# Performance work log

Measured on AMD Instinct MI355X. Metric: run time of the kernel, lower is better.

The kernel has to match this reference:

```python
import jax, jax.numpy as jnp
import numpy as np

DM = 512; DS = 16; DC = 4; DI = 1024; DI4 = 256; K = 5; NL = 2; TEMP = 0.5
B = 4; N = 1024
L4 = 2 * NL  # 2 forward layers + 2 reverse layers, stacked on leading dim


def setup_inputs() -> dict:
    key = jax.random.key(0)
    ks = jax.random.split(key, 12)
    g = lambda k, shp: jax.random.normal(k, shp, dtype=jnp.float32) * 0.02
    A0 = jnp.log(jnp.arange(1, DS + 1, dtype=jnp.float32))  # (DS,)
    return {
        "x": jax.random.normal(ks[0], (B, N, DM), dtype=jnp.float32),
        "centers_init": g(ks[1], (K, DM)),
        "in_w": g(ks[2], (L4, DM, 2 * DI)),
        "conv_w": g(ks[3], (L4, DI, DC)),
        "conv_b": jnp.zeros((L4, DI), jnp.float32),
        "xp_w": g(ks[4], (L4, DI, 2 * DS + 1)),
        "dt_w": g(ks[5], (L4, DI)),
        "dt_b": jnp.zeros((L4, DI), jnp.float32),
        "cm_w1": g(ks[6], (L4, DI4)),
        "cm_b1": jnp.zeros((L4, DI4), jnp.float32),
        "cm_w2": g(ks[7], (L4, DI4, DI)),
        "cm_b2": jnp.zeros((L4, DI), jnp.float32),
        "A_log": jnp.tile(A0[None, None, :], (L4, DI, 1)),
        "D_p": jnp.ones((L4, DI), jnp.float32),
        "out_w": g(ks[8], (L4, DI, DM)),
        "ln_g": jnp.ones((L4, DM), jnp.float32),
        "ln_b": jnp.zeros((L4, DM), jnp.float32),
        "fusion_w": g(ks[9], (2 * DM, DM)),
        "fusion_b": jnp.zeros((DM,), jnp.float32),
        "fn_g": jnp.ones((DM,), jnp.float32),
        "fn_b": jnp.zeros((DM,), jnp.float32),
    }


def _layer_norm(x, g, b, eps=1e-5):
    mu = jnp.mean(x, axis=-1, keepdims=True)
    var = jnp.mean((x - mu) ** 2, axis=-1, keepdims=True)
    return (x - mu) * jax.lax.rsqrt(var + eps) * g + b


def _cdist(a, b):
    # (B,N,C) x (B,K,C) -> (B,N,K); tiny eps for grad stability at 0
    d2 = jnp.sum((a[:, :, None, :] - b[:, None, :, :]) ** 2, axis=-1)
    return jnp.sqrt(d2 + 1e-12)


def _soft_kmeans(x, centers_init):
    Bb = x.shape[0]
    centers = jnp.broadcast_to(centers_init[None], (Bb, K, DM))
    for _ in range(3):
        dist = _cdist(x, centers)
        w = jax.nn.softmax(-dist / TEMP, axis=-1)
        num = jnp.einsum('bnk,bnc->bkc', w, x)
        den = jnp.sum(w, axis=1)[:, :, None]  # (B,K,1)
        centers = num / (den + 1e-8)
    dist = _cdist(x, centers)
    w = jax.nn.softmax(-dist / TEMP, axis=-1)
    min_dist = jnp.min(dist, axis=-1)
    importance = jax.nn.softmax(-min_dist / TEMP, axis=-1)  # softmax over N
    return centers, w, importance


def _mamba_block(x, imp, in_w, conv_w, conv_b, xp_w, dt_w, dt_b,
                 cm_w1, cm_b1, cm_w2, cm_b2, A_log, D_p, out_w, ln_g, ln_b):
    Bb, L, _ = x.shape
    res = x
    xn = _layer_norm(x, ln_g, ln_b)
    xz = xn @ in_w                      # (B,L,2*DI)
    xp, z = xz[..., :DI], xz[..., DI:]
    # causal depthwise conv1d (padding=DC-1 then truncate == left-pad)
    xc = jax.lax.conv_general_dilated(
        xp.transpose(0, 2, 1), conv_w[:, None, :], (1,), [(DC - 1, 0)],
        dimension_numbers=('NCH', 'OIH', 'NCH'), feature_group_count=DI)
    xc = (xc + conv_b[None, :, None]).transpose(0, 2, 1)  # (B,L,DI)
    xc = jax.nn.silu(xc)
    x_ssm = xc @ xp_w                   # (B,L,2*DS+1)
    draw = x_ssm[..., :1]               # (B,L,1)
    Bm = x_ssm[..., 1:1 + DS]           # (B,L,DS)
    Cm = x_ssm[..., 1 + DS:]            # (B,L,DS)
    delta = jax.nn.softplus(draw * dt_w + dt_b)  # (B,L,DI)
    h1 = jax.nn.relu(imp[..., None] * cm_w1 + cm_b1)          # (B,L,DI4)
    mod = jax.nn.sigmoid(h1 @ cm_w2 + cm_b2)                  # (B,L,DI)
    delta = delta * (1.0 + mod)
    A = -jnp.exp(A_log)                 # (DI,DS)

    def step(h, t):
        dt, bt, ct, xt = t              # (B,DI),(B,DS),(B,DS),(B,DI)
        h = jnp.exp(dt[..., None] * A) * h + (dt[..., None] * bt[:, None, :]) * xt[..., None]
        y = jnp.einsum('bdn,bn->bd', h, ct)
        return h, y

    h0 = jnp.zeros((Bb, DI, DS), x.dtype)
    xs = (delta.transpose(1, 0, 2), Bm.transpose(1, 0, 2),
          Cm.transpose(1, 0, 2), xc.transpose(1, 0, 2))
    _, ys = jax.lax.scan(step, h0, xs)  # (L,B,DI)
    y = ys.transpose(1, 0, 2) + xc * D_p
    y = y * jax.nn.silu(z)
    y = y @ out_w                       # (B,L,DM)
    return y + res                      # dropout in eval mode = identity


def _take(x, idx):
    return jnp.take_along_axis(x, idx[..., None], axis=1)


def _forward(x, centers_init, in_w, conv_w, conv_b, xp_w, dt_w, dt_b,
             cm_w1, cm_b1, cm_w2, cm_b2, A_log, D_p, out_w, ln_g, ln_b,
             fusion_w, fusion_b, fn_g, fn_b):
    centers, cw, importance = _soft_kmeans(x, centers_init)
    ca = jnp.argmax(cw, axis=-1).astype(jnp.float32)
    mw = jnp.max(cw, axis=-1)
    keys = ca * 1000.0 + (1.0 - mw)
    ridx = jnp.argsort(keys, axis=1)                     # (B,N)
    rx = _take(x, ridx)
    rimp = jnp.take_along_axis(importance, ridx, axis=1)

    def layer(i, xin, imp):
        return _mamba_block(xin, imp, in_w[i], conv_w[i], conv_b[i], xp_w[i],
                            dt_w[i], dt_b[i], cm_w1[i], cm_b1[i], cm_w2[i],
                            cm_b2[i], A_log[i], D_p[i], out_w[i], ln_g[i], ln_b[i])

    xf = rx
    for i in range(NL):
        xf = layer(i, xf, rimp)
    xb = jnp.flip(rx, axis=1)
    fimp = jnp.flip(rimp, axis=1)
    for i in range(NL, 2 * NL):
        xb = layer(i, xb, fimp)
    xb = jnp.flip(xb, axis=1)
    fused = jnp.concatenate([xf, xb], axis=-1) @ fusion_w + fusion_b
    inv = jnp.argsort(ridx, axis=1)
    restored = _take(fused, inv)
    return _layer_norm(restored, fn_g, fn_b)


def reference(x, centers_init, in_w, conv_w, conv_b, xp_w, dt_w, dt_b,
              cm_w1, cm_b1, cm_w2, cm_b2, A_log, D_p, out_w, ln_g, ln_b,
              fusion_w, fusion_b, fn_g, fn_b):
    return _forward(x, centers_init, in_w, conv_w, conv_b, xp_w, dt_w, dt_b,
                    cm_w1, cm_b1, cm_w2, cm_b2, A_log, D_p, out_w, ln_g, ln_b,
                    fusion_w, fusion_b, fn_g, fn_b)
```

## Files before the change

### kernel.cpp

```cpp
#include <hip/hip_runtime.h>
#include <math.h>

constexpr int DM = 512, DS = 16, DC = 4, DI = 1024, DI4 = 256, KC = 5;
constexpr int Bb = 4, N = 1024, L4 = 4, TT = Bb * N, TT2 = 2 * TT;
constexpr float TEMP = 0.5f;
constexpr int SEG = 16;
constexpr int SLEN = N / SEG;
constexpr int SEGU = 64;

typedef __attribute__((ext_vector_type(8))) short short8v;
typedef __attribute__((ext_vector_type(4))) float float4v;

__device__ inline ushort f2bf(float f) {
    union { float f; unsigned u; } v; v.f = f;
    unsigned r = v.u + 0x7FFFu + ((v.u >> 16) & 1u);
    return (ushort)(r >> 16);
}
__device__ inline float bf2f(ushort u) {
    union { unsigned u; float f; } v; v.u = ((unsigned)u) << 16;
    return v.f;
}
__device__ inline void gld16(const void* g, void* lds) {
    __builtin_amdgcn_global_load_lds(
        (const __attribute__((address_space(1))) unsigned int*)g,
        (__attribute__((address_space(3))) unsigned int*)lds, 16, 0, 0);
}

template <bool FINAL>
__global__ __launch_bounds__(256) void assign_k(const float* __restrict__ x,
                                                const float* __restrict__ cen0,
                                                int cbstride,
                                                float* __restrict__ wgt,
                                                float* __restrict__ mind,
                                                float* __restrict__ keys) {
    int t = blockIdx.x * 4 + (threadIdx.x >> 6);
    int b = t >> 10;
    int lane = threadIdx.x & 63;
    const float4* xr = (const float4*)(x + (size_t)t * DM);
    float4 xv0 = xr[lane], xv1 = xr[lane + 64];
    const float* cenb = cen0 + (size_t)b * cbstride;
    float d2[KC];
#pragma unroll
    for (int k = 0; k < KC; ++k) {
        const float4* cr = (const float4*)(cenb + k * DM);
        float4 c0 = cr[lane], c1 = cr[lane + 64];
        float dx = xv0.x - c0.x, dy = xv0.y - c0.y, dz = xv0.z - c0.z, dw = xv0.w - c0.w;
        float acc = dx * dx + dy * dy + dz * dz + dw * dw;
        dx = xv1.x - c1.x; dy = xv1.y - c1.y; dz = xv1.z - c1.z; dw = xv1.w - c1.w;
        acc += dx * dx + dy * dy + dz * dz + dw * dw;
        d2[k] = acc;
    }
#pragma unroll
    for (int k = 0; k < KC; ++k)
        for (int off = 32; off > 0; off >>= 1) d2[k] += __shfl_xor(d2[k], off);
    if (lane == 0) {
        float dist[KC], logit[KC], e[KC];
        float lm = -1e30f;
        for (int k = 0; k < KC; ++k) {
            dist[k] = sqrtf(d2[k] + 1e-12f);
            logit[k] = -dist[k] / TEMP;
            lm = fmaxf(lm, logit[k]);
        }
        float s = 0.f;
        for (int k = 0; k < KC; ++k) { e[k] = expf(logit[k] - lm); s += e[k]; }
        float inv = 1.f / s;
        for (int k = 0; k < KC; ++k) wgt[t * KC + k] = e[k] * inv;
        if (FINAL) {
            float md = dist[0];
            for (int k = 1; k < KC; ++k) md = fminf(md, dist[k]);
            int ca = 0; float best = e[0] * inv;
            for (int k = 1; k < KC; ++k) {
                float wv = e[k] * inv;
                if (wv > best) { best = wv; ca = k; }
            }
            mind[t] = md;
            keys[t] = (float)ca * 1000.0f + (1.0f - best);
        }
    }
}

__global__ __launch_bounds__(512) void updp_k(const float* __restrict__ x,
                                              const float* __restrict__ wgt,
                                              float* __restrict__ part,
                                              float* __restrict__ denp) {
    int blk = blockIdx.x;
    int b = blk >> 6, seg = blk & 63;
    int c = threadIdx.x;
    constexpr int TSEG = N / SEGU;
    __shared__ float sw[TSEG][KC];
    int n0 = seg * TSEG;
    if (c < TSEG * KC) sw[c / KC][c % KC] = wgt[((size_t)(b << 10) + n0 + c / KC) * KC + c % KC];
    __syncthreads();
    const float* xb = x + ((size_t)(b << 10) + n0) * DM + c;
    float acc[KC] = {};
    for (int n = 0; n < TSEG; ++n) {
        float xv = xb[(size_t)n * DM];
#pragma unroll
        for (int k = 0; k < KC; ++k) acc[k] = fmaf(sw[n][k], xv, acc[k]);
    }
#pragma unroll
    for (int k = 0; k < KC; ++k)
        part[(((size_t)b * KC + k) * SEGU + seg) * DM + c] = acc[k];
    if (c < KC) {
        float dn = 0.f;
        for (int n = 0; n < TSEG; ++n) dn += sw[n][c];
        denp[((size_t)b * KC + c) * SEGU + seg] = dn;
    }
}

__global__ __launch_bounds__(512) void updr_k(const float* __restrict__ part,
                                              const float* __restrict__ denp,
                                              float* __restrict__ centers) {
    int bk = blockIdx.x;
    int c = threadIdx.x;
    const float* pb = part + (size_t)bk * SEGU * DM + c;
    float acc = 0.f;
    for (int g = 0; g < SEGU; ++g) acc += pb[(size_t)g * DM];
    __shared__ float sden;
    if (c == 0) {
        float dn = 0.f;
        const float* db = denp + (size_t)bk * SEGU;
        for (int g = 0; g < SEGU; ++g) dn += db[g];
        sden = dn;
    }
    __syncthreads();
    centers[(size_t)bk * DM + c] = acc / (sden + 1e-8f);
}

__global__ __launch_bounds__(1024) void sortimp_k(const float* __restrict__ keys,
                                                  const float* __restrict__ mind,
                                                  int* __restrict__ ridx,
                                                  float* __restrict__ imp) {
    __shared__ unsigned long long a[1024];
    int tid = threadIdx.x;
    if (blockIdx.x < 4) {
        int b = blockIdx.x;
        unsigned int kb = __float_as_uint(keys[b * N + tid]);
        a[tid] = ((unsigned long long)kb << 32) | (unsigned int)tid;
        __syncthreads();
        for (int k = 2; k <= 1024; k <<= 1) {
            for (int j = k >> 1; j > 0; j >>= 1) {
                int ixj = tid ^ j;
                if (ixj > tid) {
                    unsigned long long x0 = a[tid], x1 = a[ixj];
                    bool up = ((tid & k) == 0);
                    bool sw = up ? (x0 > x1) : (x0 < x1);
                    if (sw) { a[tid] = x1; a[ixj] = x0; }
                }
                __syncthreads();
            }
        }
        ridx[b * N + tid] = (int)(a[tid] & 0xffffffffu);
    } else {
        int b = blockIdx.x - 4;
        float* red = (float*)a;
        float v = -mind[b * N + tid] / TEMP;
        red[tid] = v; __syncthreads();
        for (int s = 512; s > 0; s >>= 1) { if (tid < s) red[tid] = fmaxf(red[tid], red[tid + s]); __syncthreads(); }
        float m = red[0]; __syncthreads();
        float e = expf(v - m);
        red[tid] = e; __syncthreads();
        for (int s = 512; s > 0; s >>= 1) { if (tid < s) red[tid] += red[tid + s]; __syncthreads(); }
        imp[b * N + tid] = e / red[0];
    }
}

__global__ __launch_bounds__(512) void gather_k(const float* __restrict__ x,
                                                const float* __restrict__ imp,
                                                const int* __restrict__ ridx,
                                                float* __restrict__ act0,
                                                float* __restrict__ impc) {
    int t = blockIdx.x;
    int b = t >> 10, j = t & (N - 1);
    int r = ridx[t];
    int c = threadIdx.x;
    float v = x[((size_t)(b << 10) + r) * DM + c];
    act0[(size_t)t * DM + c] = v;
    act0[((size_t)TT + (b << 10) + (N - 1 - j)) * DM + c] = v;
    if (c == 0) {
        float iv = imp[(b << 10) + r];
        impc[t] = iv;
        impc[TT + (b << 10) + (N - 1 - j)] = iv;
    }
}

__device__ inline void tconv_body(const float* __restrict__ src, ushort* __restrict__ dst,
                                  int R, int C, int c0, int r0, float* tile ) {
    int tx = threadIdx.x & 31, ty = threadIdx.x >> 5;
#pragma unroll
    for (int j = 0; j < 4; ++j)
        tile[(ty + j * 8) * 33 + tx] = src[(size_t)(r0 + ty + j * 8) * C + c0 + tx];
    __syncthreads();
#pragma unroll
    for (int j = 0; j < 4; ++j)
        dst[(size_t)(c0 + ty + j * 8) * R + r0 + tx] = f2bf(tile[tx * 33 + ty + j * 8]);
}

__global__ __launch_bounds__(256) void prep_k(const float* __restrict__ in_w,
                                              const float* __restrict__ cm_w2,
                                              const float* __restrict__ out_w,
                                              const float* __restrict__ fusion_w,
                                              const float* __restrict__ xp_w,
                                              ushort* __restrict__ inwT, ushort* __restrict__ cmw2T,
                                              ushort* __restrict__ outwT, ushort* __restrict__ fusT,
                                              ushort* __restrict__ xpwT) {
    __shared__ float lds[256 * 33];
    int bx = blockIdx.x;
    if (bx < 4096) {
        int l = bx >> 10, i = bx & 1023;
        tconv_body(in_w + (size_t)l * DM * 2 * DI, inwT + (size_t)l * 2 * DI * DM,
                   DM, 2 * DI, (i & 63) * 32, (i >> 6) * 32, lds);
        return;
    }
    bx -= 4096;
    if (bx < 1024) {
        int l = bx >> 8, i = bx & 255;
        tconv_body(cm_w2 + (size_t)l * DI4 * DI, cmw2T + (size_t)l * DI * DI4,
                   DI4, DI, (i & 31) * 32, (i >> 5) * 32, lds);
        return;
    }
    bx -= 1024;
    if (bx < 2048) {
        int l = bx >> 9, i = bx & 511;
        tconv_body(out_w + (size_t)l * DI * DM, outwT + (size_t)l * DM * DI,
                   DI, DM, (i & 15) * 32, (i >> 4) * 32, lds);
        return;
    }
    bx -= 2048;
    if (bx < 512) {
        tconv_body(fusion_w, fusT, 2 * DM, DM, (bx & 15) * 32, (bx >> 4) * 32, lds);
        return;
    }
    bx -= 512;
    {
        int l = bx >> 2, chunk = bx & 3;
        int c0 = chunk * 256, tid = threadIdx.x;
        const float* src = xp_w + (size_t)l * DI * 33 + (size_t)c0 * 33;
        for (int i = tid; i < 256 * 33; i += 256) lds[i] = src[i];
        __syncthreads();
        ushort* dst = xpwT + (size_t)l * 128 * DI;
        for (int j = 0; j < 128; ++j) {
            ushort v = (j < 33) ? f2bf(lds[tid * 33 + j]) : (ushort)0;
            dst[(size_t)j * DI + c0 + tid] = v;
        }
    }
}

__global__ __launch_bounds__(256) void tpose33_k(const float* __restrict__ xssmP,
                                                 float* __restrict__ xssmT) {
    int t0 = blockIdx.x * 64, tid = threadIdx.x;
    __shared__ float lds[64 * 129];
    const float* src = xssmP + (size_t)t0 * 128;
    const size_t PS = (size_t)TT2 * 128;
    for (int i = tid; i < 64 * 128; i += 256) {
        float v = src[i] + src[i + PS] + src[i + 2 * PS] + src[i + 3 * PS];
        lds[(i >> 7) * 129 + (i & 127)] = v;
    }
    __syncthreads();
    int tk = tid & 63, jq = tid >> 6;
    for (int j = jq; j < 33; j += 4)
        xssmT[(size_t)j * TT2 + t0 + tk] = lds[tk * 129 + j];
}

__global__ __launch_bounds__(256) void ln_k(const float* __restrict__ xin,
                                            const float* __restrict__ ln_g,
                                            const float* __restrict__ ln_b,
                                            int lA, int lB,
                                            ushort* __restrict__ out) {
    int t = blockIdx.x * 4 + (threadIdx.x >> 6);
    int lane = threadIdx.x & 63;
    int l = (t < TT) ? lA : lB;
    const float* g = ln_g + (size_t)l * DM;
    const float* bt = ln_b + (size_t)l * DM;
    const float4* xr = (const float4*)(xin + (size_t)t * DM);
    float4 v0 = xr[lane * 2], v1 = xr[lane * 2 + 1];
    float s = ((v0.x + v0.y) + (v0.z + v0.w)) + ((v1.x + v1.y) + (v1.z + v1.w));
#pragma unroll
    for (int off = 32; off > 0; off >>= 1) s += __shfl_xor(s, off);
    float mu = s * (1.f / DM);
    float d0 = v0.x - mu, d1 = v0.y - mu, d2 = v0.z - mu, d3 = v0.w - mu;
    float d4 = v1.x - mu, d5 = v1.y - mu, d6 = v1.z - mu, d7 = v1.w - mu;
    float q = ((d0 * d0 + d1 * d1) + (d2 * d2 + d3 * d3)) + ((d4 * d4 + d5 * d5) + (d6 * d6 + d7 * d7));
#pragma unroll
    for (int off = 32; off > 0; off >>= 1) q += __shfl_xor(q, off);
    float rs = rsqrtf(q * (1.f / DM) + 1e-5f);
    const float4* gr = (const float4*)g;
    const float4* br = (const float4*)bt;
    float4 g0 = gr[lane * 2], g1 = gr[lane * 2 + 1];
    float4 b0 = br[lane * 2], b1 = br[lane * 2 + 1];
    uint4 pk;
    pk.x = (unsigned)f2bf(d0 * rs * g0.x + b0.x) | ((unsigned)f2bf(d1 * rs * g0.y + b0.y) << 16);
    pk.y = (unsigned)f2bf(d2 * rs * g0.z + b0.z) | ((unsigned)f2bf(d3 * rs * g0.w + b0.w) << 16);
    pk.z = (unsigned)f2bf(d4 * rs * g1.x + b1.x) | ((unsigned)f2bf(d5 * rs * g1.y + b1.y) << 16);
    pk.w = (unsigned)f2bf(d6 * rs * g1.z + b1.z) | ((unsigned)f2bf(d7 * rs * g1.w + b1.w) << 16);
    *(uint4*)(out + (size_t)t * DM + lane * 8) = pk;
}

template <bool BF16OUT>
__global__ __launch_bounds__(256) void mgemm_k(const ushort* __restrict__ A, int lda,
                                               const ushort* __restrict__ BtA,
                                               const ushort* __restrict__ BtB, int ldb,
                                               const float* __restrict__ biasA,
                                               const float* __restrict__ biasB,
                                               const float* __restrict__ add, int ldadd,
                                               void* __restrict__ Cout, int ldc, int Kdim,
                                               size_t czs) {
    __shared__ short8v As[2][128 * 4];
    __shared__ short8v Bs[2][128 * 4];
    int tid = threadIdx.x;
    int lane = tid & 63, wid = tid >> 6;
    int row0 = blockIdx.y * 128, col0 = blockIdx.x * 128;
    const ushort* Bt = (row0 < TT || !BtB) ? BtA : BtB;
    const float* bias = (row0 < TT || !BtB) ? biasA : biasB;
    int wr = (wid >> 1) * 64, wc = (wid & 1) * 64;
    float4v acc[4][4];
#pragma unroll
    for (int i = 0; i < 4; ++i)
#pragma unroll
        for (int j = 0; j < 4; ++j)
#pragma unroll
            for (int r = 0; r < 4; ++r) acc[i][j][r] = 0.f;

    int rq0 = wid * 32 + (lane >> 2);
    int rq1 = rq0 + 16;
    int clds = lane & 3;
    int cs0 = clds ^ ((rq0 >> 1) & 3);
    int cs1 = clds ^ ((rq1 >> 1) & 3);
    const ushort* aSrc0 = A + (size_t)(row0 + rq0) * lda + cs0 * 8;
    const ushort* aSrc1 = A + (size_t)(row0 + rq1) * lda + cs1 * 8;
    const ushort* bSrc0 = Bt + (size_t)(col0 + rq0) * ldb + cs0 * 8;
    const ushort* bSrc1 = Bt + (size_t)(col0 + rq1) * ldb + cs1 * 8;

    int fr = lane & 15, kg = lane >> 4;
    int sf = kg ^ ((fr >> 1) & 3);

    int kslice = Kdim / (int)gridDim.z;
    int kbeg = (int)blockIdx.z * kslice;
    int T = kslice / 32;

    gld16(aSrc0 + kbeg, &As[0][wid * 128]);
    gld16(aSrc1 + kbeg, &As[0][wid * 128 + 64]);
    gld16(bSrc0 + kbeg, &Bs[0][wid * 128]);
    gld16(bSrc1 + kbeg, &Bs[0][wid * 128 + 64]);
    __syncthreads();
    int cur = 0;
    for (int i = 0; i < T; ++i) {
        if (i + 1 < T) {
            int kn = kbeg + (i + 1) * 32;
            gld16(aSrc0 + kn, &As[cur ^ 1][wid * 128]);
            gld16(aSrc1 + kn, &As[cur ^ 1][wid * 128 + 64]);
            gld16(bSrc0 + kn, &Bs[cur ^ 1][wid * 128]);
            gld16(bSrc1 + kn, &Bs[cur ^ 1][wid * 128 + 64]);
        }
        short8v af[4], bf[4];
#pragma unroll
        for (int mb = 0; mb < 4; ++mb) af[mb] = As[cur][(wr + mb * 16 + fr) * 4 + sf];
#pragma unroll
        for (int nb = 0; nb < 4; ++nb) bf[nb] = Bs[cur][(wc + nb * 16 + fr) * 4 + sf];
#pragma unroll
        for (int mb = 0; mb < 4; ++mb)
#pragma unroll
            for (int nb = 0; nb < 4; ++nb)
                acc[mb][nb] = __builtin_amdgcn_mfma_f32_16x16x32_bf16(af[mb], bf[nb], acc[mb][nb], 0, 0, 0);
        __syncthreads();
        cur ^= 1;
    }
    ushort* cu = (ushort*)Cout + (size_t)blockIdx.z * czs;
    float* cf = (float*)Cout + (size_t)blockIdx.z * czs;
#pragma unroll
    for (int mb = 0; mb < 4; ++mb) {
        int r_ = row0 + wr + mb * 16 + kg * 4;
#pragma unroll
        for (int nb = 0; nb < 4; ++nb) {
            int c_ = col0 + wc + nb * 16 + fr;
            float bz = bias ? bias[c_] : 0.f;
#pragma unroll
            for (int r = 0; r < 4; ++r) {
                float o = acc[mb][nb][r] + bz;
                if (add) o += add[(size_t)(r_ + r) * ldadd + c_];
                if (BF16OUT) cu[(size_t)(r_ + r) * ldc + c_] = f2bf(o);
                else         cf[(size_t)(r_ + r) * ldc + c_] = o;
            }
        }
    }
}

__global__ __launch_bounds__(256) void mgemmH_k(const float* __restrict__ impc,
                                                const float* __restrict__ cm_w1,
                                                const float* __restrict__ cm_b1,
                                                const ushort* __restrict__ cmw2T,
                                                const float* __restrict__ cm_b2,
                                                int lA, int lB,
                                                ushort* __restrict__ Cout, int ldc) {
    __shared__ short8v As[2][128 * 4];
    __shared__ short8v Bs[2][128 * 4];
    int tid = threadIdx.x;
    int lane = tid & 63, wid = tid >> 6;
    int row0 = blockIdx.y * 128, col0 = blockIdx.x * 128;
    int l = (row0 < TT) ? lA : lB;
    const float* w1 = cm_w1 + (size_t)l * DI4;
    const float* b1 = cm_b1 + (size_t)l * DI4;
    const ushort* Bt = cmw2T + (size_t)l * DI * DI4;
    const float* bias = cm_b2 + (size_t)l * DI;
    int wr = (wid >> 1) * 64, wc = (wid & 1) * 64;
    float4v acc[4][4];
#pragma unroll
    for (int i = 0; i < 4; ++i)
#pragma unroll
        for (int j = 0; j < 4; ++j)
#pragma unroll
            for (int r = 0; r < 4; ++r) acc[i][j][r] = 0.f;

    int rq0 = wid * 32 + (lane >> 2);
    int rq1 = rq0 + 16;
    int clds = lane & 3;
    int cs0 = clds ^ ((rq0 >> 1) & 3);
    int cs1 = clds ^ ((rq1 >> 1) & 3);
    float imp0 = impc[row0 + rq0];
    float imp1 = impc[row0 + rq1];
    const ushort* bSrc0 = Bt + (size_t)(col0 + rq0) * DI4 + cs0 * 8;
    const ushort* bSrc1 = Bt + (size_t)(col0 + rq1) * DI4 + cs1 * 8;

    int fr = lane & 15, kg = lane >> 4;
    int sf = kg ^ ((fr >> 1) & 3);

    auto mkA = [&](int k0, float impv, int cs, short8v* dst) {
        float4 w0 = *(const float4*)(w1 + k0 + cs * 8);
        float4 w4 = *(const float4*)(w1 + k0 + cs * 8 + 4);
        float4 bq0 = *(const float4*)(b1 + k0 + cs * 8);
        float4 bq4 = *(const float4*)(b1 + k0 + cs * 8 + 4);
        short8v p;
        p[0] = (short)f2bf(fmaxf(fmaf(impv, w0.x, bq0.x), 0.f));
        p[1] = (short)f2bf(fmaxf(fmaf(impv, w0.y, bq0.y), 0.f));
        p[2] = (short)f2bf(fmaxf(fmaf(impv, w0.z, bq0.z), 0.f));
        p[3] = (short)f2bf(fmaxf(fmaf(impv, w0.w, bq0.w), 0.f));
        p[4] = (short)f2bf(fmaxf(fmaf(impv, w4.x, bq4.x), 0.f));
        p[5] = (short)f2bf(fmaxf(fmaf(impv, w4.y, bq4.y), 0.f));
        p[6] = (short)f2bf(fmaxf(fmaf(impv, w4.z, bq4.z), 0.f));
        p[7] = (short)f2bf(fmaxf(fmaf(impv, w4.w, bq4.w), 0.f));
        *dst = p;
    };

    mkA(0, imp0, cs0, &As[0][rq0 * 4 + clds]);
    mkA(0, imp1, cs1, &As[0][rq1 * 4 + clds]);
    gld16(bSrc0, &Bs[0][wid * 128]);
    gld16(bSrc1, &Bs[0][wid * 128 + 64]);
    __syncthreads();
    int cur = 0;
    constexpr int T = DI4 / 32;
    for (int i = 0; i < T; ++i) {
        if (i + 1 < T) {
            int kn = (i + 1) * 32;
            mkA(kn, imp0, cs0, &As[cur ^ 1][rq0 * 4 + clds]);
            mkA(kn, imp1, cs1, &As[cur ^ 1][rq1 * 4 + clds]);
            gld16(bSrc0 + kn, &Bs[cur ^ 1][wid * 128]);
            gld16(bSrc1 + kn, &Bs[cur ^ 1][wid * 128 + 64]);
        }
        short8v af[4], bf[4];
#pragma unroll
        for (int mb = 0; mb < 4; ++mb) af[mb] = As[cur][(wr + mb * 16 + fr) * 4 + sf];
#pragma unroll
        for (int nb = 0; nb < 4; ++nb) bf[nb] = Bs[cur][(wc + nb * 16 + fr) * 4 + sf];
#pragma unroll
        for (int mb = 0; mb < 4; ++mb)
#pragma unroll
            for (int nb = 0; nb < 4; ++nb)
                acc[mb][nb] = __builtin_amdgcn_mfma_f32_16x16x32_bf16(af[mb], bf[nb], acc[mb][nb], 0, 0, 0);
        __syncthreads();
        cur ^= 1;
    }
#pragma unroll
    for (int mb = 0; mb < 4; ++mb) {
        int r_ = row0 + wr + mb * 16 + kg * 4;
#pragma unroll
        for (int nb = 0; nb < 4; ++nb) {
            int c_ = col0 + wc + nb * 16 + fr;
            float bz = bias[c_];
#pragma unroll
            for (int r = 0; r < 4; ++r)
                Cout[(size_t)(r_ + r) * ldc + c_] = f2bf(acc[mb][nb][r] + bz);
        }
    }
}

__global__ __launch_bounds__(256) void conv_k(const ushort* __restrict__ xz,
                                              const float* __restrict__ conv_w,
                                              const float* __restrict__ conv_b,
                                              int lA, int lB,
                                              ushort* __restrict__ xcb) {
    int gid = blockIdx.x * 256 + threadIdx.x;
    int p = gid & (DI / 2 - 1);
    int d = p * 2;
    int t = gid >> 9;
    int n = t & (N - 1);
    int l = (t < TT) ? lA : lB;
    const float* cw = conv_w + (size_t)l * DI * DC;
    const float* cb = conv_b + (size_t)l * DI;
    float acc0 = cb[d], acc1 = cb[d + 1];
    const ushort* base = xz + (size_t)t * (2 * DI) + d;
    float4 w0 = *(const float4*)(cw + d * DC);
    float4 w1 = *(const float4*)(cw + (d + 1) * DC);
    float wk0[4] = {w0.x, w0.y, w0.z, w0.w};
    float wk1[4] = {w1.x, w1.y, w1.z, w1.w};
#pragma unroll
    for (int k = 0; k < DC; ++k) {
        int nn = n - (DC - 1) + k;
        if (nn >= 0) {
            unsigned u = *(const unsigned*)(base + (long)(nn - n) * (2 * DI));
            acc0 = fmaf(bf2f((ushort)(u & 0xffff)), wk0[k], acc0);
            acc1 = fmaf(bf2f((ushort)(u >> 16)), wk1[k], acc1);
        }
    }
    float s0 = acc0 / (1.f + __expf(-acc0));
    float s1 = acc1 / (1.f + __expf(-acc1));
    unsigned o = (unsigned)f2bf(s0) | ((unsigned)f2bf(s1) << 16);
    *(unsigned*)(xcb + (size_t)t * DI + d) = o;
}

__global__ __launch_bounds__(256) void scanA_k(const ushort* __restrict__ modl,
                                               const ushort* __restrict__ xcb,
                                               const float* __restrict__ xssmT,
                                               const float* __restrict__ Alog0,
                                               const float* __restrict__ dtw0,
                                               const float* __restrict__ dtb0,
                                               int lA, int lB,
                                               float* __restrict__ delf,
                                               float* __restrict__ hloc,
                                               float* __restrict__ Pp) {
    int blk = blockIdx.x;
    int seg = blk & 15;
    int dblk = (blk >> 4) & 63;
    int b = blk >> 10;
    int l = (b < 4) ? lA : lB;
    const float* Alog = Alog0 + (size_t)l * DI * DS;
    const float* dtw = dtw0 + (size_t)l * DI;
    const float* dtb = dtb0 + (size_t)l * DI;
    int d0 = dblk * 16;
    int tid = threadIdx.x;
    int lane = tid & 63, wave = tid >> 6;
    int s = lane & 15, dd = lane >> 4;
    int dl = wave * 4 + dd, d = d0 + dl;
    float A = -__expf(Alog[d * DS + s]);
    size_t tokbase = (size_t)b * N + (size_t)seg * SLEN;

    __shared__ float sdl[16][68];
    __shared__ float sxc[16][68];
    __shared__ float sBv[16][68];

    int lc = tid & 15, lr = tid >> 4;
    float dtwv = dtw[d0 + lc], dtbv = dtb[d0 + lc];
    const ushort* mbase = modl + tokbase * DI + d0 + lc;
    const ushort* xbase = xcb + tokbase * DI + d0 + lc;
    const float* drow = xssmT + tokbase;
    const float* Brow = xssmT + (size_t)(1 + lc) * TT2 + tokbase;
#pragma unroll
    for (int q = 0; q < 4; ++q) {
        int tok = q * 16 + lr;
        float mo   = bf2f(mbase[(size_t)tok * DI]);
        float draw = drow[tok];
        float xcv  = bf2f(xbase[(size_t)tok * DI]);
        float Bv   = Brow[tok];
        float a = draw * dtwv + dtbv;
        float sp = (a > 20.f) ? a : log1pf(__expf(a));
        float mod = 1.f / (1.f + __expf(-mo));
        float dlv = sp * (1.f + mod);
        sdl[lc][tok] = dlv;
        delf[(tokbase + tok) * DI + d0 + lc] = dlv;
        sxc[lc][tok] = xcv;
        sBv[lc][tok] = Bv;
    }
    __syncthreads();
    float h = 0.f, P = 1.f;
#pragma unroll
    for (int g = 0; g < 8; ++g) {
        float4 dl4a = *(const float4*)&sdl[dl][g * 8];
        float4 dl4b = *(const float4*)&sdl[dl][g * 8 + 4];
        float4 xc4a = *(const float4*)&sxc[dl][g * 8];
        float4 xc4b = *(const float4*)&sxc[dl][g * 8 + 4];
        float4 B4a  = *(const float4*)&sBv[s][g * 8];
        float4 B4b  = *(const float4*)&sBv[s][g * 8 + 4];
        float dlt[8] = {dl4a.x, dl4a.y, dl4a.z, dl4a.w, dl4b.x, dl4b.y, dl4b.z, dl4b.w};
        float xcv[8] = {xc4a.x, xc4a.y, xc4a.z, xc4a.w, xc4b.x, xc4b.y, xc4b.z, xc4b.w};
        float Bv8[8] = {B4a.x, B4a.y, B4a.z, B4a.w, B4b.x, B4b.y, B4b.z, B4b.w};
        float a8[8], b8[8];
#pragma unroll
        for (int j = 0; j < 8; ++j) {
            a8[j] = __expf(dlt[j] * A);
            b8[j] = (dlt[j] * Bv8[j]) * xcv[j];
        }
#pragma unroll
        for (int j = 0; j < 8; ++j) { h = fmaf(a8[j], h, b8[j]); P *= a8[j]; }
    }
    size_t idx = (size_t)blk * 256 + tid;
    hloc[idx] = h;
    Pp[idx] = P;
}

__global__ __launch_bounds__(256) void scanB_k(const float* __restrict__ hloc,
                                               const float* __restrict__ Pp,
                                               float* __restrict__ h0g) {
    int blk = blockIdx.x;
    int tid = threadIdx.x;
    size_t base = (size_t)blk * SEG * 256 + tid;
    float h = 0.f;
    for (int g = 0; g < SEG; ++g) {
        size_t i = base + (size_t)g * 256;
        h0g[i] = h;
        h = fmaf(Pp[i], h, hloc[i]);
    }
}

__global__ __launch_bounds__(256) void scanC_k(const float* __restrict__ delf,
                                               const ushort* __restrict__ xcb,
                                               const float* __restrict__ xssmT,
                                               const float* __restrict__ Alog0,
                                               const float* __restrict__ Dp0,
                                               const ushort* __restrict__ xz,
                                               int lA, int lB,
                                               const float* __restrict__ h0g,
                                               ushort* __restrict__ y) {
    int blk = blockIdx.x;
    int seg = blk & 15;
    int dblk = (blk >> 4) & 63;
    int b = blk >> 10;
    int l = (b < 4) ? lA : lB;
    const float* Alog = Alog0 + (size_t)l * DI * DS;
    const float* Dp = Dp0 + (size_t)l * DI;
    int d0 = dblk * 16;
    int tid = threadIdx.x;
    int lane = tid & 63, wave = tid >> 6;
    int s = lane & 15, dd = lane >> 4;
    int dl = wave * 4 + dd, d = d0 + dl;
    float A = -__expf(Alog[d * DS + s]);
    size_t tokbase = (size_t)b * N + (size_t)seg * SLEN;

    __shared__ float sdl[16][68];
    __shared__ float sxc[16][68];
    __shared__ float sBv[16][68];
    __shared__ float sCv[16][68];
    __shared__ float szv[16][68];
    __shared__ float sP[16][16][17];

    int lc = tid & 15, lr = tid >> 4;
    float dpv_lc = Dp[d0 + lc];
    const float* dbase = delf + tokbase * DI + d0 + lc;
    const ushort* xbase = xcb + tokbase * DI + d0 + lc;
    const ushort* zbase = xz + tokbase * (2 * DI) + DI + d0 + lc;
    const float* Brow = xssmT + (size_t)(1 + lc) * TT2 + tokbase;
    const float* Crow = xssmT + (size_t)(1 + DS + lc) * TT2 + tokbase;
#pragma unroll
    for (int q = 0; q < 4; ++q) {
        int tok = q * 16 + lr;
        sdl[lc][tok] = dbase[(size_t)tok * DI];
        sxc[lc][tok] = bf2f(xbase[(size_t)tok * DI]);
        sBv[lc][tok] = Brow[tok];
        sCv[lc][tok] = Crow[tok];
        szv[lc][tok] = bf2f(zbase[(size_t)tok * (2 * DI)]);
    }
    __syncthreads();
    float h = h0g[(size_t)blk * 256 + tid];
    for (int g = 0; g < 4; ++g) {
#pragma unroll
        for (int half = 0; half < 2; ++half) {
            int t0 = g * 16 + half * 8;
            float4 dl4a = *(const float4*)&sdl[dl][t0];
            float4 dl4b = *(const float4*)&sdl[dl][t0 + 4];
            float4 xc4a = *(const float4*)&sxc[dl][t0];
            float4 xc4b = *(const float4*)&sxc[dl][t0 + 4];
            float4 B4a  = *(const float4*)&sBv[s][t0];
            float4 B4b  = *(const float4*)&sBv[s][t0 + 4];
            float4 C4a  = *(const float4*)&sCv[s][t0];
            float4 C4b  = *(const float4*)&sCv[s][t0 + 4];
            float dlt[8] = {dl4a.x, dl4a.y, dl4a.z, dl4a.w, dl4b.x, dl4b.y, dl4b.z, dl4b.w};
            float xcv[8] = {xc4a.x, xc4a.y, xc4a.z, xc4a.w, xc4b.x, xc4b.y, xc4b.z, xc4b.w};
            float Bv8[8] = {B4a.x, B4a.y, B4a.z, B4a.w, B4b.x, B4b.y, B4b.z, B4b.w};
            float Cv8[8] = {C4a.x, C4a.y, C4a.z, C4a.w, C4b.x, C4b.y, C4b.z, C4b.w};
            float a8[8], b8[8];
#pragma unroll
            for (int j = 0; j < 8; ++j) {
                a8[j] = __expf(dlt[j] * A);
                b8[j] = (dlt[j] * Bv8[j]) * xcv[j];
            }
#pragma unroll
            for (int j = 0; j < 8; ++j) {
                h = fmaf(a8[j], h, b8[j]);
                sP[half * 8 + j][dl][s] = h * Cv8[j];
            }
        }
        __syncthreads();
        {
            int t = g * 16 + lr;
            float ssum = 0.f;
#pragma unroll
            for (int s2 = 0; s2 < 16; ++s2) ssum += sP[lr][lc][s2];
            float xcv = sxc[lc][t];
            float zv  = szv[lc][t];
            float sg = 1.f / (1.f + __expf(-zv));
            y[(tokbase + t) * DI + d0 + lc] = f2bf((ssum + xcv * dpv_lc) * (zv * sg));
        }
        __syncthreads();
    }
}

__global__ __launch_bounds__(256) void concat_k(const float* __restrict__ act0,
                                                ushort* __restrict__ cat) {
    int gid = blockIdx.x * 256 + threadIdx.x;
    int t = gid >> 9;
    int c = gid & (DM - 1);
    int b = t >> 10, j = t & (N - 1);
    cat[(size_t)t * (2 * DM) + c] = f2bf(act0[(size_t)t * DM + c]);
    cat[(size_t)t * (2 * DM) + DM + c] =
        f2bf(act0[((size_t)TT + (b << 10) + (N - 1 - j)) * DM + c]);
}

__global__ __launch_bounds__(256) void final_k(const float* __restrict__ fus,
                                               const int* __restrict__ ridx,
                                               const float* __restrict__ g,
                                               const float* __restrict__ bt,
                                               float* __restrict__ out) {
    int t = blockIdx.x, tid = threadIdx.x;
    int b = t >> 10;
    int r = ridx[t];
    const float* xr = fus + (size_t)t * DM;
    __shared__ float red[256];
    float v0 = xr[tid], v1 = xr[tid + 256];
    red[tid] = v0 + v1; __syncthreads();
    for (int st = 128; st > 0; st >>= 1) { if (tid < st) red[tid] += red[tid + st]; __syncthreads(); }
    float mu = red[0] * (1.f / DM); __syncthreads();
    float d0 = v0 - mu, d1 = v1 - mu;
    red[tid] = d0 * d0 + d1 * d1; __syncthreads();
    for (int st = 128; st > 0; st >>= 1) { if (tid < st) red[tid] += red[tid + st]; __syncthreads(); }
    float rs = rsqrtf(red[0] * (1.f / DM) + 1e-5f);
    float* orow = out + ((size_t)(b << 10) + r) * DM;
    orow[tid] = d0 * rs * g[tid] + bt[tid];
    orow[tid + 256] = d1 * rs * g[tid + 256] + bt[tid + 256];
}

extern "C" void kernel_launch(void* const* d_in, const int* in_sizes, int n_in,
                              void* d_out, int out_size, void* d_ws, size_t ws_size,
                              hipStream_t stream) {
    const float* x            = (const float*)d_in[0];
    const float* centers_init = (const float*)d_in[1];
    const float* in_w         = (const float*)d_in[2];
    const float* conv_w       = (const float*)d_in[3];
    const float* conv_b       = (const float*)d_in[4];
    const float* xp_w         = (const float*)d_in[5];
    const float* dt_w         = (const float*)d_in[6];
    const float* dt_b         = (const float*)d_in[7];
    const float* cm_w1        = (const float*)d_in[8];
    const float* cm_b1        = (const float*)d_in[9];
    const float* cm_w2        = (const float*)d_in[10];
    const float* cm_b2        = (const float*)d_in[11];
    const float* A_log        = (const float*)d_in[12];
    const float* D_p          = (const float*)d_in[13];
    const float* out_w        = (const float*)d_in[14];
    const float* ln_g         = (const float*)d_in[15];
    const float* ln_b         = (const float*)d_in[16];
    const float* fusion_w     = (const float*)d_in[17];
    const float* fusion_b     = (const float*)d_in[18];
    const float* fn_g         = (const float*)d_in[19];
    const float* fn_b         = (const float*)d_in[20];

    float* W = (float*)d_ws;
    size_t off = 0;
    auto alloc = [&](size_t n) { float* p = W + off; off += (n + 15) & ~(size_t)15; return p; };
    auto allocU = [&](size_t n) { ushort* p = (ushort*)(W + off); off += ((n + 1) / 2 + 15) & ~(size_t)15; return p; };
    float* centers = alloc((size_t)Bb * KC * DM);
    float* wgt     = alloc((size_t)TT * KC);
    float* mind    = alloc(TT);
    float* keys    = alloc(TT);
    float* imp     = alloc(TT);
    float* impc    = alloc(TT2);
    float* denp    = alloc((size_t)Bb * KC * SEGU);
    float* act0    = alloc((size_t)TT2 * DM);
    float* act1    = alloc((size_t)TT2 * DM);
    float* xssmT   = alloc((size_t)TT2 * 33);
    float* delf    = alloc((size_t)TT2 * DI);
    float* hloc    = alloc((size_t)8 * 64 * SEG * 256);
    float* Pp      = alloc((size_t)8 * 64 * SEG * 256);
    float* h0g     = alloc((size_t)8 * 64 * SEG * 256);
    ushort* xz     = allocU((size_t)TT2 * 2 * DI);
    ushort* modl   = allocU((size_t)TT2 * DI);
    ushort* yb     = allocU((size_t)TT2 * DI);
    ushort* xcb    = allocU((size_t)TT2 * DI);
    ushort* inwT   = allocU((size_t)L4 * 2 * DI * DM);
    ushort* cmw2T  = allocU((size_t)L4 * DI * DI4);
    ushort* outwT  = allocU((size_t)L4 * DM * DI);
    ushort* fusT   = allocU((size_t)DM * 2 * DM);
    ushort* xpwT   = allocU((size_t)L4 * 128 * DI);
    int* ridx = (int*)(W + off); off += TT;
    float* part = (float*)modl;
    float* xssmP = hloc;
    ushort* xnb = yb;
    float* fus = act1;

    prep_k<<<7696, 256, 0, stream>>>(in_w, cm_w2, out_w, fusion_w, xp_w,
                                     inwT, cmw2T, outwT, fusT, xpwT);

    for (int it = 0; it < 3; ++it) {
        if (it == 0) assign_k<false><<<TT / 4, 256, 0, stream>>>(x, centers_init, 0, wgt, nullptr, nullptr);
        else         assign_k<false><<<TT / 4, 256, 0, stream>>>(x, centers, KC * DM, wgt, nullptr, nullptr);
        updp_k<<<Bb * SEGU, 512, 0, stream>>>(x, wgt, part, denp);
        updr_k<<<Bb * KC, 512, 0, stream>>>(part, denp, centers);
    }
    assign_k<true><<<TT / 4, 256, 0, stream>>>(x, centers, KC * DM, wgt, mind, keys);
    sortimp_k<<<8, 1024, 0, stream>>>(keys, mind, ridx, imp);
    gather_k<<<TT, 512, 0, stream>>>(x, imp, ridx, act0, impc);

    float* pin[2]  = {act0, act1};
    float* pout[2] = {act1, act0};
    for (int pr = 0; pr < 2; ++pr) {
        int lA = pr, lB = pr + 2;
        float* actin = pin[pr];
        float* actout = pout[pr];
        ln_k<<<TT2 / 4, 256, 0, stream>>>(actin, ln_g, ln_b, lA, lB, xnb);
        {
            dim3 g(2 * DI / 128, TT2 / 128, 1);
            mgemm_k<true><<<g, 256, 0, stream>>>(xnb, DM,
                inwT + (size_t)lA * 2 * DI * DM, inwT + (size_t)lB * 2 * DI * DM, DM,
                nullptr, nullptr, nullptr, 0, xz, 2 * DI, DM, 0);
        }
        conv_k<<<(TT2 * DI / 2) / 256, 256, 0, stream>>>(xz, conv_w, conv_b, lA, lB, xcb);
        {
            dim3 g(1, TT2 / 128, 4);
            mgemm_k<false><<<g, 256, 0, stream>>>(xcb, DI,
                xpwT + (size_t)lA * 128 * DI, xpwT + (size_t)lB * 128 * DI, DI,
                nullptr, nullptr, nullptr, 0, xssmP, 128, DI, (size_t)TT2 * 128);
        }
        tpose33_k<<<TT2 / 64, 256, 0, stream>>>(xssmP, xssmT);
        mgemmH_k<<<dim3(DI / 128, TT2 / 128), 256, 0, stream>>>(impc, cm_w1, cm_b1, cmw2T, cm_b2,
                                                                lA, lB, modl, DI);
        scanA_k<<<8 * 64 * SEG, 256, 0, stream>>>(modl, xcb, xssmT, A_log, dt_w, dt_b,
                                                  lA, lB, delf, hloc, Pp);
        scanB_k<<<8 * 64, 256, 0, stream>>>(hloc, Pp, h0g);
        scanC_k<<<8 * 64 * SEG, 256, 0, stream>>>(delf, xcb, xssmT, A_log, D_p, xz,
                                                  lA, lB, h0g, yb);
        {
            dim3 g(DM / 128, TT2 / 128, 1);
            mgemm_k<false><<<g, 256, 0, stream>>>(yb, DI,
                outwT + (size_t)lA * DM * DI, outwT + (size_t)lB * DM * DI, DI,
                nullptr, nullptr, actin, DM, actout, DM, DI, 0);
        }
    }

    ushort* catb = xz;
    concat_k<<<(TT * DM) / 256, 256, 0, stream>>>(act0, catb);
    {
        dim3 g(DM / 128, TT / 128, 1);
        mgemm_k<false><<<g, 256, 0, stream>>>(catb, 2 * DM, fusT, nullptr, 2 * DM,
                                              fusion_b, nullptr, nullptr, 0, fus, DM, 2 * DM, 0);
    }
    final_k<<<TT, 256, 0, stream>>>(fus, ridx, fn_g, fn_b, (float*)d_out);
}
```

Baseline: 619.0 us.

## Fuse delta computation into modulation GEMM epilogue and rework scanC reduction

The modulation GEMM epilogue now computes the full delta (softplus of dt projection times one plus sigmoid of the modulation) and writes it directly as fp32, removing the bf16 modl intermediate. scanA then only loads the precomputed delta instead of recomputing it and writing it back. Separately, scanC processes 8 tokens per group with a halved shared sP buffer and splits the 16-state sum across lane pairs with a shuffle. This trades a bf16 write plus read for an fp32 write, and doubles the number of barrier rounds in scanC.

```diff
diff --git a/kernel.cpp b/kernel.cpp
--- a/kernel.cpp
+++ b/kernel.cpp
@@ -390,8 +390,11 @@
                                                 const float* __restrict__ cm_b1,
                                                 const ushort* __restrict__ cmw2T,
                                                 const float* __restrict__ cm_b2,
+                                                const float* __restrict__ dt_w,
+                                                const float* __restrict__ dt_b,
+                                                const float* __restrict__ xssmT,
                                                 int lA, int lB,
-                                                ushort* __restrict__ Cout, int ldc) {
+                                                float* __restrict__ delf) {
     __shared__ short8v As[2][128 * 4];
     __shared__ short8v Bs[2][128 * 4];
     int tid = threadIdx.x;
@@ -402,6 +405,8 @@
     const float* b1 = cm_b1 + (size_t)l * DI4;
     const ushort* Bt = cmw2T + (size_t)l * DI * DI4;
     const float* bias = cm_b2 + (size_t)l * DI;
+    const float* dtw = dt_w + (size_t)l * DI;
+    const float* dtb = dt_b + (size_t)l * DI;
     int wr = (wid >> 1) * 64, wc = (wid & 1) * 64;
     float4v acc[4][4];
 #pragma unroll
@@ -472,13 +477,24 @@
 #pragma unroll
     for (int mb = 0; mb < 4; ++mb) {
         int r_ = row0 + wr + mb * 16 + kg * 4;
+        float draw0 = xssmT[r_ + 0];
+        float draw1 = xssmT[r_ + 1];
+        float draw2 = xssmT[r_ + 2];
+        float draw3 = xssmT[r_ + 3];
+        float draw[4] = {draw0, draw1, draw2, draw3};
 #pragma unroll
         for (int nb = 0; nb < 4; ++nb) {
             int c_ = col0 + wc + nb * 16 + fr;
             float bz = bias[c_];
-#pragma unroll
-            for (int r = 0; r < 4; ++r)
-                Cout[(size_t)(r_ + r) * ldc + c_] = f2bf(acc[mb][nb][r] + bz);
+            float dw = dtw[c_], db = dtb[c_];
+#pragma unroll
+            for (int r = 0; r < 4; ++r) {
+                float mo = acc[mb][nb][r] + bz;
+                float a = fmaf(draw[r], dw, db);
+                float sp = (a > 20.f) ? a : log1pf(__expf(a));
+                float mod = 1.f / (1.f + __expf(-mo));
+                delf[(size_t)(r_ + r) * DI + c_] = sp * (1.f + mod);
+            }
         }
     }
 }
@@ -517,14 +533,11 @@
     *(unsigned*)(xcb + (size_t)t * DI + d) = o;
 }
 
-__global__ __launch_bounds__(256) void scanA_k(const ushort* __restrict__ modl,
+__global__ __launch_bounds__(256) void scanA_k(const float* __restrict__ delf,
                                                const ushort* __restrict__ xcb,
                                                const float* __restrict__ xssmT,
                                                const float* __restrict__ Alog0,
-                                               const float* __restrict__ dtw0,
-                                               const float* __restrict__ dtb0,
                                                int lA, int lB,
-                                               float* __restrict__ delf,
                                                float* __restrict__ hloc,
                                                float* __restrict__ Pp) {
     int blk = blockIdx.x;
@@ -533,8 +546,6 @@
     int b = blk >> 10;
     int l = (b < 4) ? lA : lB;
     const float* Alog = Alog0 + (size_t)l * DI * DS;
-    const float* dtw = dtw0 + (size_t)l * DI;
-    const float* dtb = dtb0 + (size_t)l * DI;
     int d0 = dblk * 16;
     int tid = threadIdx.x;
     int lane = tid & 63, wave = tid >> 6;
@@ -548,26 +559,15 @@
     __shared__ float sBv[16][68];
 
     int lc = tid & 15, lr = tid >> 4;
-    float dtwv = dtw[d0 + lc], dtbv = dtb[d0 + lc];
-    const ushort* mbase = modl + tokbase * DI + d0 + lc;
+    const float* dbase = delf + tokbase * DI + d0 + lc;
     const ushort* xbase = xcb + tokbase * DI + d0 + lc;
-    const float* drow = xssmT + tokbase;
     const float* Brow = xssmT + (size_t)(1 + lc) * TT2 + tokbase;
 #pragma unroll
     for (int q = 0; q < 4; ++q) {
         int tok = q * 16 + lr;
-        float mo   = bf2f(mbase[(size_t)tok * DI]);
-        float draw = drow[tok];
-        float xcv  = bf2f(xbase[(size_t)tok * DI]);
-        float Bv   = Brow[tok];
-        float a = draw * dtwv + dtbv;
-        float sp = (a > 20.f) ? a : log1pf(__expf(a));
-        float mod = 1.f / (1.f + __expf(-mo));
-        float dlv = sp * (1.f + mod);
-        sdl[lc][tok] = dlv;
-        delf[(tokbase + tok) * DI + d0 + lc] = dlv;
-        sxc[lc][tok] = xcv;
-        sBv[lc][tok] = Bv;
+        sdl[lc][tok] = dbase[(size_t)tok * DI];
+        sxc[lc][tok] = bf2f(xbase[(size_t)tok * DI]);
+        sBv[lc][tok] = Brow[tok];
     }
     __syncthreads();
     float h = 0.f, P = 1.f;
@@ -639,7 +639,7 @@
     __shared__ float sBv[16][68];
     __shared__ float sCv[16][68];
     __shared__ float szv[16][68];
-    __shared__ float sP[16][16][17];
+    __shared__ float sP[8][16][17];
 
     int lc = tid & 15, lr = tid >> 4;
     float dpv_lc = Dp[d0 + lc];
@@ -659,10 +659,10 @@
     }
     __syncthreads();
     float h = h0g[(size_t)blk * 256 + tid];
-    for (int g = 0; g < 4; ++g) {
-#pragma unroll
-        for (int half = 0; half < 2; ++half) {
-            int t0 = g * 16 + half * 8;
+    int j8 = tid >> 5, rlc = (tid >> 1) & 15, rhalf = tid & 1;
+    for (int g = 0; g < 8; ++g) {
+        {
+            int t0 = g * 8;
             float4 dl4a = *(const float4*)&sdl[dl][t0];
             float4 dl4b = *(const float4*)&sdl[dl][t0 + 4];
             float4 xc4a = *(const float4*)&sxc[dl][t0];
@@ -684,19 +684,22 @@
 #pragma unroll
             for (int j = 0; j < 8; ++j) {
                 h = fmaf(a8[j], h, b8[j]);
-                sP[half * 8 + j][dl][s] = h * Cv8[j];
+                sP[j][dl][s] = h * Cv8[j];
             }
         }
         __syncthreads();
         {
-            int t = g * 16 + lr;
+            int t = g * 8 + j8;
             float ssum = 0.f;
 #pragma unroll
-            for (int s2 = 0; s2 < 16; ++s2) ssum += sP[lr][lc][s2];
-            float xcv = sxc[lc][t];
-            float zv  = szv[lc][t];
-            float sg = 1.f / (1.f + __expf(-zv));
-            y[(tokbase + t) * DI + d0 + lc] = f2bf((ssum + xcv * dpv_lc) * (zv * sg));
+            for (int s2 = 0; s2 < 8; ++s2) ssum += sP[j8][rlc][rhalf * 8 + s2];
+            ssum += __shfl_xor(ssum, 1);
+            if (rhalf == 0) {
+                float xcv = sxc[rlc][t];
+                float zv  = szv[rlc][t];
+                float sg = 1.f / (1.f + __expf(-zv));
+                y[(tokbase + t) * DI + d0 + rlc] = f2bf((ssum + xcv * dpv_lc) * (zv * sg));
+            }
         }
         __syncthreads();
     }
@@ -780,7 +783,6 @@
     float* Pp      = alloc((size_t)8 * 64 * SEG * 256);
     float* h0g     = alloc((size_t)8 * 64 * SEG * 256);
     ushort* xz     = allocU((size_t)TT2 * 2 * DI);
-    ushort* modl   = allocU((size_t)TT2 * DI);
     ushort* yb     = allocU((size_t)TT2 * DI);
     ushort* xcb    = allocU((size_t)TT2 * DI);
     ushort* inwT   = allocU((size_t)L4 * 2 * DI * DM);
@@ -789,7 +791,7 @@
     ushort* fusT   = allocU((size_t)DM * 2 * DM);
     ushort* xpwT   = allocU((size_t)L4 * 128 * DI);
     int* ridx = (int*)(W + off); off += TT;
-    float* part = (float*)modl;
+    float* part = delf;
     float* xssmP = hloc;
     ushort* xnb = yb;
     float* fus = act1;
@@ -829,9 +831,8 @@
         }
         tpose33_k<<<TT2 / 64, 256, 0, stream>>>(xssmP, xssmT);
         mgemmH_k<<<dim3(DI / 128, TT2 / 128), 256, 0, stream>>>(impc, cm_w1, cm_b1, cmw2T, cm_b2,
-                                                                lA, lB, modl, DI);
-        scanA_k<<<8 * 64 * SEG, 256, 0, stream>>>(modl, xcb, xssmT, A_log, dt_w, dt_b,
-                                                  lA, lB, delf, hloc, Pp);
+                                                                dt_w, dt_b, xssmT, lA, lB, delf);
+        scanA_k<<<8 * 64 * SEG, 256, 0, stream>>>(delf, xcb, xssmT, A_log, lA, lB, hloc, Pp);
         scanB_k<<<8 * 64, 256, 0, stream>>>(hloc, Pp, h0g);
         scanC_k<<<8 * 64 * SEG, 256, 0, stream>>>(delf, xcb, xssmT, A_log, D_p, xz,
                                                   lA, lB, h0g, yb);
```

After: 817.1 us. 1.32x slower.
